# Kernel tuning notes

Hardware: AMD Instinct MI355X
Metric: run time of the kernel (lower is better)

Reference implementation:

```python
import math
import jax, jax.numpy as jnp
import numpy as np

B, H, L = 8, 512, 4096
N = 64 // 2  # d_state//2 complex pairs
DT_MIN, DT_MAX = 1e-3, 0.1


def setup_inputs() -> dict:
    key = jax.random.key(0)
    k_u, k_dt, k_C, k_D, k_W = jax.random.split(key, 5)
    u = jax.random.normal(k_u, (B, H, L), dtype=jnp.float32)
    log_dt = jax.random.uniform(k_dt, (H,), dtype=jnp.float32) * (
        math.log(DT_MAX) - math.log(DT_MIN)) + math.log(DT_MIN)
    log_A_real = jnp.log(0.5 * jnp.ones((H, N), dtype=jnp.float32))
    A_imag = math.pi * jnp.broadcast_to(jnp.arange(N, dtype=jnp.float32), (H, N))
    C = jax.random.normal(k_C, (H, N, 2), dtype=jnp.float32)  # view_as_real of cfloat
    D = jax.random.normal(k_D, (H,), dtype=jnp.float32)
    W_out = jax.random.normal(k_W, (2 * H, H), dtype=jnp.float32) * 0.05  # 1x1 conv weight
    b_out = jnp.zeros((2 * H,), dtype=jnp.float32)
    return {"u": u, "log_dt": log_dt, "log_A_real": log_A_real, "A_imag": A_imag,
            "C": C, "D": D, "W_out": W_out, "b_out": b_out}


def _ssm_kernel(log_dt, log_A_real, A_imag, C, length):
    dt = jnp.exp(log_dt)                             # (H,)
    A = -jnp.exp(log_A_real) + 1j * A_imag           # (H,N) complex
    dtA = A * dt[:, None]                            # (H,N)
    l = jnp.arange(length, dtype=jnp.float32)
    K = jnp.exp(dtA[:, :, None] * l)                 # (H,N,L) complex Vandermonde
    Cc = C[..., 0] + 1j * C[..., 1]                  # (H,N)
    Cs = Cc * (jnp.exp(dtA) - 1.0) / A               # (H,N)
    return 2.0 * jnp.einsum('hn,hnl->hl', Cs, K).real  # (H,L) real kernel


def reference(u, log_dt, log_A_real, A_imag, C, D, W_out, b_out):
    length = u.shape[-1]
    k = _ssm_kernel(log_dt, log_A_real, A_imag, C, length)  # (H,L)
    n_fft = 2 * length
    k_f = jnp.fft.rfft(k, n=n_fft)                   # (H, L+1)
    u_f = jnp.fft.rfft(u, n=n_fft)                   # (B,H,L+1)
    y = jnp.fft.irfft(u_f * k_f, n=n_fft)[..., :length]  # FFT convolution
    y = y + u * D[:, None]                           # D skip connection
    y = jax.nn.gelu(y, approximate=False)            # torch nn.GELU = exact erf
    y = jnp.einsum('oh,bhl->bol', W_out, y) + b_out[:, None]  # 1x1 conv
    a, b = jnp.split(y, 2, axis=-2)                  # GLU over channel dim
    return a * jax.nn.sigmoid(b)
```

## Files before the change

kernel.cpp:

```cpp
#include <hip/hip_runtime.h>
#include <math.h>

constexpr int cB = 8, cH = 512, cL = 4096, cN = 32;
constexpr int cG = 32, cLC = 128;
constexpr int cHN = cH * cN;

constexpr size_t OF_RR  = 0;
constexpr size_t OF_RI  = (size_t)cHN;
constexpr size_t OF_RPR = (size_t)2*cHN;
constexpr size_t OF_RPI = (size_t)3*cHN;
constexpr size_t OF_C2R = (size_t)4*cHN;
constexpr size_t OF_C2I = (size_t)5*cHN;
constexpr size_t OF_DR  = (size_t)6*cHN;
constexpr size_t OF_DI  = (size_t)7*cHN;
constexpr size_t OF_K   = (size_t)8*cHN;
constexpr size_t OF_WP  = OF_K + (size_t)512*128;
constexpr size_t OF_A   = OF_WP + (size_t)1024*512/2;
constexpr size_t OF_V   = OF_A + (size_t)512*128*192/2;
constexpr size_t OF_XP  = OF_V + (size_t)512*64*128/2;
constexpr size_t OF_G   = OF_XP + (size_t)512*256*64/2;

typedef __bf16 bf16x8 __attribute__((ext_vector_type(8)));
typedef float  f32x4  __attribute__((ext_vector_type(4)));

static __device__ __forceinline__ ushort f2bf(float x) {
    unsigned u = __float_as_uint(x);
    unsigned r = (u + 0x7fffu + ((u >> 16) & 1u)) >> 16;
    return (ushort)r;
}
static __device__ __forceinline__ float bf2f(ushort v) {
    return __uint_as_float(((unsigned)v) << 16);
}
static __device__ __forceinline__ unsigned pk2(float a, float b) {
    return (unsigned)f2bf(a) | ((unsigned)f2bf(b) << 16);
}
static __device__ __forceinline__ float gelu(float v) {
    return 0.5f * v * (1.0f + erff(v * 0.70710678118654752f));
}

__global__ void k_consts(const float* __restrict__ log_dt,
                         const float* __restrict__ log_A_real,
                         const float* __restrict__ A_imag,
                         const float* __restrict__ Cin,
                         float* __restrict__ ws)
{
    int tid = blockIdx.x * 256 + threadIdx.x;
    if (tid >= cHN) return;
    int h = tid >> 5;
    float dt = expf(log_dt[h]);
    float Ar = -expf(log_A_real[tid]);
    float Ai = A_imag[tid];
    float dr = dt * Ar, di = dt * Ai;
    float er = expf(dr);
    float rr = er * cosf(di), ri = er * sinf(di);
    float erL = expf(dr * (float)cLC);
    float diL = di * (float)cLC;
    float rpr = erL * cosf(diL), rpi = erL * sinf(diL);
    float cr = Cin[2*tid], ci = Cin[2*tid+1];
    float nr = rr - 1.0f, ni = ri;
    float inv = 1.0f / (Ar*Ar + Ai*Ai);
    float wr = (nr*Ar + ni*Ai) * inv;
    float wi = (ni*Ar - nr*Ai) * inv;
    float csr = cr*wr - ci*wi;
    float csi = cr*wi + ci*wr;
    ws[OF_RR  + tid] = rr;  ws[OF_RI  + tid] = ri;
    ws[OF_RPR + tid] = rpr; ws[OF_RPI + tid] = rpi;
    ws[OF_C2R + tid] = 2.0f*csr; ws[OF_C2I + tid] = 2.0f*csi;
    ws[OF_DR  + tid] = dr;  ws[OF_DI  + tid] = di;
}

__global__ void k_pack_w(const float* __restrict__ W, ushort* __restrict__ Wp)
{
    int idx = blockIdx.x * 256 + threadIdx.x;
    int base = idx * 4;
    int m = base >> 9;
    int k = base & 511;
    int src = (m & 1) ? (512 + (m >> 1)) : (m >> 1);
    float4 v = *(const float4*)&W[(size_t)src * 512 + k];
    ushort4 o;
    o.x = f2bf(v.x); o.y = f2bf(v.y); o.z = f2bf(v.z); o.w = f2bf(v.w);
    *(ushort4*)&Wp[base] = o;
}

__global__ void k_vmat(const float* __restrict__ ws, ushort* __restrict__ wsu)
{
    int tid = blockIdx.x * 256 + threadIdx.x;
    int h = tid >> 5, n = tid & 31;
    float dr = ws[OF_DR + tid], di = ws[OF_DI + tid];
    float e127 = expf(dr * 127.f), a127 = di * 127.f;
    float pr = e127 * cosf(a127), pi_ = e127 * sinf(a127);
    float rie = expf(-dr);
    float rc = rie * cosf(di), rs = -rie * sinf(di);
    ushort* vre = wsu + 2*OF_V + ((size_t)h*64 + n) * 128;
    ushort* vim = wsu + 2*OF_V + ((size_t)h*64 + 32 + n) * 128;
    for (int j4 = 0; j4 < 128; j4 += 4) {
        ushort4 r4, i4;
        #pragma unroll
        for (int e = 0; e < 4; ++e) {
            ((ushort*)&r4)[e] = f2bf(pr);
            ((ushort*)&i4)[e] = f2bf(pi_);
            float npr = pr*rc - pi_*rs;
            float npi = pr*rs + pi_*rc;
            pr = npr; pi_ = npi;
        }
        *(ushort4*)&vre[j4] = r4;
        *(ushort4*)&vim[j4] = i4;
    }
}

__global__ void k_emat(const float* __restrict__ ws, float* __restrict__ wsf,
                       ushort* __restrict__ wsu)
{
    int tid = blockIdx.x * 256 + threadIdx.x;
    int h = tid >> 7, l = tid & 127;
    float fl = (float)l, fl1 = (float)(l + 1);
    const float* dr_ = ws + OF_DR + (size_t)h*32;
    const float* di_ = ws + OF_DI + (size_t)h*32;
    const float* c2r_ = ws + OF_C2R + (size_t)h*32;
    const float* c2i_ = ws + OF_C2I + (size_t)h*32;
    ushort* rowA = wsu + 2*OF_A + ((size_t)h*128 + l) * 192;
    float kacc = 0.f;
    for (int n4 = 0; n4 < 32; n4 += 4) {
        ushort4 prq, npq;
        #pragma unroll
        for (int e = 0; e < 4; ++e) {
            int n = n4 + e;
            float dr = dr_[n], di = di_[n], c2r = c2r_[n], c2i = c2i_[n];
            float e0 = expf(dr * fl), a0 = di * fl;
            float c0 = cosf(a0), s0 = sinf(a0);
            kacc += e0 * (c2r*c0 - c2i*s0);
            float e1 = expf(dr * fl1), a1 = di * fl1;
            float c1 = cosf(a1), s1 = sinf(a1);
            ((ushort*)&prq)[e] = f2bf(e1 * (c2r*c1 - c2i*s1));
            ((ushort*)&npq)[e] = f2bf(-e1 * (c2r*s1 + c2i*c1));
        }
        *(ushort4*)&rowA[128 + n4] = prq;
        *(ushort4*)&rowA[160 + n4] = npq;
    }
    wsf[OF_K + (size_t)h*128 + l] = kacc;
}

__global__ void k_build_T(const float* __restrict__ wsf, const float* __restrict__ Dvec,
                          ushort* __restrict__ wsu)
{
    __shared__ float kv[256];
    int t = threadIdx.x;
    int tid = blockIdx.x * 256 + t;
    int h = tid >> 7, l = tid & 127;
    kv[t] = wsf[OF_K + (size_t)blockIdx.x * 256 + t];
    __syncthreads();
    const float* krow = kv + ((t >> 7) << 7);
    float Dh = Dvec[h];
    ushort* row = wsu + 2*OF_A + ((size_t)h*128 + l) * 192;
    for (int j8 = 0; j8 < 128; j8 += 8) {
        uint4 q;
        unsigned w[4];
        #pragma unroll
        for (int p = 0; p < 4; ++p) {
            int j0 = j8 + 2*p, j1 = j0 + 1;
            float v0 = (j0 <= l) ? krow[l - j0] : 0.f;
            float v1 = (j1 <= l) ? krow[l - j1] : 0.f;
            if (j0 == l) v0 += Dh;
            if (j1 == l) v1 += Dh;
            w[p] = pk2(v0, v1);
        }
        q.x = w[0]; q.y = w[1]; q.z = w[2]; q.w = w[3];
        *(uint4*)&row[j8] = q;
    }
}

__global__ __launch_bounds__(256) void k_state_gemm(const float* __restrict__ u,
                                                    const ushort* __restrict__ wsu,
                                                    ushort* __restrict__ xp)
{
    __shared__ ushort Vs[64 * 136];
    __shared__ ushort Bs[256 * 40];
    const int t = threadIdx.x;
    const int h = blockIdx.x;
    const int wn = t >> 6, lane = t & 63;
    const int lm = lane & 15, q = lane >> 4;

    {
        int idx = t * 32;
        int row = idx >> 7, kk = idx & 127;
        const ushort* src = wsu + 2*OF_V + ((size_t)h*64 + row) * 128 + kk;
        uint4 v0 = *(const uint4*)&src[0],  v1 = *(const uint4*)&src[8];
        uint4 v2 = *(const uint4*)&src[16], v3 = *(const uint4*)&src[24];
        ushort* d = (ushort*)Vs + row * 136 + kk;
        *(uint4*)&d[0] = v0; *(uint4*)&d[8] = v1;
        *(uint4*)&d[16] = v2; *(uint4*)&d[24] = v3;
    }

    const int b = t >> 5, c = t & 31;
    f32x4 acc[4][4];
    #pragma unroll
    for (int i = 0; i < 4; ++i)
        #pragma unroll
        for (int j = 0; j < 4; ++j) acc[i][j] = (f32x4){0.f,0.f,0.f,0.f};

    for (int k0 = 0; k0 < 128; k0 += 32) {
        const float* up = u + ((size_t)(b*cH + h)) * cL + (size_t)c*128 + k0;
        float4 f[8];
        #pragma unroll
        for (int e = 0; e < 8; ++e) f[e] = *(const float4*)&up[4*e];
        __syncthreads();
        ushort* d = (ushort*)Bs + t * 40;
        #pragma unroll
        for (int e = 0; e < 4; ++e) {
            uint4 w;
            w.x = pk2(f[2*e].x, f[2*e].y);   w.y = pk2(f[2*e].z, f[2*e].w);
            w.z = pk2(f[2*e+1].x, f[2*e+1].y); w.w = pk2(f[2*e+1].z, f[2*e+1].w);
            *(uint4*)&d[8*e] = w;
        }
        __syncthreads();
        bf16x8 af[4], bfr[4];
        #pragma unroll
        for (int mi = 0; mi < 4; ++mi)
            af[mi] = *(const bf16x8*)&Vs[(16*mi + lm) * 136 + k0 + 8*q];
        #pragma unroll
        for (int ni = 0; ni < 4; ++ni)
            bfr[ni] = *(const bf16x8*)&Bs[(64*wn + 16*ni + lm) * 40 + 8*q];
        #pragma unroll
        for (int mi = 0; mi < 4; ++mi)
            #pragma unroll
            for (int ni = 0; ni < 4; ++ni)
                acc[mi][ni] = __builtin_amdgcn_mfma_f32_16x16x32_bf16(af[mi], bfr[ni], acc[mi][ni], 0,0,0);
    }
    #pragma unroll
    for (int mi = 0; mi < 4; ++mi)
        #pragma unroll
        for (int ni = 0; ni < 4; ++ni) {
            int col = 64*wn + 16*ni + lm;
            int comp = 16*mi + 4*q;
            ushort4 st;
            st.x = f2bf(acc[mi][ni][0]); st.y = f2bf(acc[mi][ni][1]);
            st.z = f2bf(acc[mi][ni][2]); st.w = f2bf(acc[mi][ni][3]);
            *(ushort4*)&xp[((size_t)h*256 + col) * 64 + comp] = st;
        }
}

__global__ __launch_bounds__(256) void k_scan2(const float* __restrict__ ws,
                                               ushort* __restrict__ xp)
{
    int tid = blockIdx.x * 256 + threadIdx.x;
    int n  = tid & 31;
    int bh = tid >> 5;
    int h  = bh & (cH - 1);
    int b  = bh >> 9;
    float rpr = ws[OF_RPR + (size_t)h*32 + n];
    float rpi = ws[OF_RPI + (size_t)h*32 + n];
    float Xr = 0.f, Xi = 0.f;
    ushort* base = xp + ((size_t)h*256 + (size_t)b*32) * 64 + n;
    for (int c = 0; c < cG; ++c) {
        ushort* p = base + (size_t)c * 64;
        float sr = bf2f(p[0]), si = bf2f(p[32]);
        p[0]  = f2bf(Xr);
        p[32] = f2bf(Xi);
        float nXr = fmaf(rpr, Xr, fmaf(-rpi, Xi, sr));
        float nXi = fmaf(rpr, Xi, fmaf(rpi, Xr, si));
        Xr = nXr; Xi = nXi;
    }
}

__global__ __launch_bounds__(256) void k_conv(const float* __restrict__ u,
                                              const ushort* __restrict__ wsu,
                                              ushort* __restrict__ g)
{
    __shared__ ushort As[128 * 40];
    __shared__ ushort Bs[128 * 40];
    const int t = threadIdx.x;
    const int ctile = blockIdx.x;
    const int h = blockIdx.y;
    const int wave = t >> 6, lane = t & 63;
    const int wm = wave & 1, wn = wave >> 1;
    const int lm = lane & 15, q = lane >> 4;

    const int arow = t & 127, ah = t >> 7;
    const int col = arow, half = ah;
    const int gc = ctile * 128 + col;
    const int ub = gc >> 5, uc = gc & 31;

    const ushort* Ab = wsu + 2*OF_A + ((size_t)h*128 + arow) * 192;
    const ushort* xpB = wsu + 2*OF_XP + ((size_t)h*256 + gc) * 64;

    f32x4 acc[4][4];
    #pragma unroll
    for (int i = 0; i < 4; ++i)
        #pragma unroll
        for (int j = 0; j < 4; ++j) acc[i][j] = (f32x4){0.f,0.f,0.f,0.f};

    for (int k0 = 0; k0 < 192; k0 += 32) {
        uint4 a0 = *(const uint4*)&Ab[k0 + 16*ah];
        uint4 a1 = *(const uint4*)&Ab[k0 + 16*ah + 8];
        uint4 b0, b1;
        if (k0 < 128) {
            const float* up = u + ((size_t)(ub*cH + h)) * cL + (size_t)uc*128 + k0 + 16*half;
            float4 f0 = *(const float4*)&up[0],  f1 = *(const float4*)&up[4];
            float4 f2 = *(const float4*)&up[8],  f3 = *(const float4*)&up[12];
            b0.x = pk2(f0.x,f0.y); b0.y = pk2(f0.z,f0.w);
            b0.z = pk2(f1.x,f1.y); b0.w = pk2(f1.z,f1.w);
            b1.x = pk2(f2.x,f2.y); b1.y = pk2(f2.z,f2.w);
            b1.z = pk2(f3.x,f3.y); b1.w = pk2(f3.z,f3.w);
        } else {
            const ushort* xs = xpB + (k0 - 128) + 16*half;
            b0 = *(const uint4*)&xs[0];
            b1 = *(const uint4*)&xs[8];
        }
        __syncthreads();
        *(uint4*)&As[arow*40 + 16*ah]     = a0;
        *(uint4*)&As[arow*40 + 16*ah + 8] = a1;
        *(uint4*)&Bs[col*40 + 16*half]     = b0;
        *(uint4*)&Bs[col*40 + 16*half + 8] = b1;
        __syncthreads();
        bool skip = (wm == 0) && (k0 == 64 || k0 == 96);
        if (!skip) {
            bf16x8 af[4], bfr[4];
            #pragma unroll
            for (int mi = 0; mi < 4; ++mi)
                af[mi] = *(const bf16x8*)&As[(64*wm + 16*mi + lm) * 40 + 8*q];
            #pragma unroll
            for (int ni = 0; ni < 4; ++ni)
                bfr[ni] = *(const bf16x8*)&Bs[(64*wn + 16*ni + lm) * 40 + 8*q];
            #pragma unroll
            for (int mi = 0; mi < 4; ++mi)
                #pragma unroll
                for (int ni = 0; ni < 4; ++ni)
                    acc[mi][ni] = __builtin_amdgcn_mfma_f32_16x16x32_bf16(af[mi], bfr[ni], acc[mi][ni], 0,0,0);
        }
    }
    #pragma unroll
    for (int ni = 0; ni < 4; ++ni) {
        int ocol = ctile*128 + 64*wn + 16*ni + lm;
        int ob = ocol >> 5, oc = ocol & 31;
        ushort* grow = g + ((size_t)(ob*cH + h)) * cL + (size_t)oc*128;
        #pragma unroll
        for (int mi = 0; mi < 4; ++mi) {
            int l = 64*wm + 16*mi + 4*q;
            ushort4 st;
            st.x = f2bf(gelu(acc[mi][ni][0]));
            st.y = f2bf(gelu(acc[mi][ni][1]));
            st.z = f2bf(gelu(acc[mi][ni][2]));
            st.w = f2bf(gelu(acc[mi][ni][3]));
            *(ushort4*)&grow[l] = st;
        }
    }
}

constexpr int LDK = 40;
__global__ __launch_bounds__(256) void k_gemm_mfma(const ushort* __restrict__ Wp,
                                                   const float* __restrict__ bias,
                                                   const ushort* __restrict__ gbf,
                                                   float* __restrict__ out)
{
    __shared__ ushort As[128 * LDK];
    __shared__ ushort Bs[128 * LDK];
    const int t    = threadIdx.x;
    const int l0   = blockIdx.x * 128;
    const int by   = blockIdx.y;
    const int b    = blockIdx.z;
    const int wave = t >> 6, lane = t & 63;
    const int wm   = wave & 1, wn = wave >> 1;
    const int lm   = lane & 15, q = lane >> 4;

    const int arow = t & 127;
    const int ah   = t >> 7;
    const int lq = t & 15, kp = t >> 4;
    const int ko = kp >> 2;
    const int kr = (2 * kp) & 7;

    const ushort* gB = gbf + (size_t)b * ((size_t)cH * cL);
    const ushort* wRow = Wp + (size_t)(by * 128 + arow) * 512 + ah * 16;

    f32x4 acc[4][4];
    #pragma unroll
    for (int i = 0; i < 4; ++i)
        #pragma unroll
        for (int j = 0; j < 4; ++j)
            acc[i][j] = (f32x4){0.f, 0.f, 0.f, 0.f};

    for (int k0 = 0; k0 < cH; k0 += 32) {
        uint4 wa0 = *(const uint4*)&wRow[k0];
        uint4 wa1 = *(const uint4*)&wRow[k0 + 8];
        uint4 g0  = *(const uint4*)&gB[(size_t)(k0 + 2*kp)     * cL + l0 + 8*lq];
        uint4 g1  = *(const uint4*)&gB[(size_t)(k0 + 2*kp + 1) * cL + l0 + 8*lq];
        __syncthreads();
        *(uint4*)&As[arow * LDK + 16*ah]     = wa0;
        *(uint4*)&As[arow * LDK + 16*ah + 8] = wa1;
        {
            unsigned ua[4] = {g0.x, g0.y, g0.z, g0.w};
            unsigned ub[4] = {g1.x, g1.y, g1.z, g1.w};
            #pragma unroll
            for (int e = 0; e < 4; ++e) {
                unsigned w0 = (ua[e] & 0xffffu) | (ub[e] << 16);
                unsigned w1 = (ua[e] >> 16)     | (ub[e] & 0xffff0000u);
                int lr0 = 8*lq + 2*e;
                int c0  = ((ko ^ (lq & 3)) << 3) + kr;
                *(unsigned*)&Bs[lr0 * LDK + c0]       = w0;
                *(unsigned*)&Bs[(lr0 + 1) * LDK + c0] = w1;
            }
        }
        __syncthreads();
        bf16x8 af[4], bf[4];
        #pragma unroll
        for (int mi = 0; mi < 4; ++mi) {
            int row = 64*wm + 16*mi + lm;
            af[mi] = *(const bf16x8*)&As[row * LDK + (q << 3)];
        }
        #pragma unroll
        for (int ni = 0; ni < 4; ++ni) {
            int row = 64*wn + 16*ni + lm;
            int kx  = (row >> 3) & 3;
            bf[ni] = *(const bf16x8*)&Bs[row * LDK + ((q ^ kx) << 3)];
        }
        #pragma unroll
        for (int mi = 0; mi < 4; ++mi)
            #pragma unroll
            for (int ni = 0; ni < 4; ++ni)
                acc[mi][ni] = __builtin_amdgcn_mfma_f32_16x16x32_bf16(af[mi], bf[ni], acc[mi][ni], 0, 0, 0);
    }

    const int obase = by * 64 + 32 * wm;
    #pragma unroll
    for (int mi = 0; mi < 4; ++mi) {
        #pragma unroll
        for (int p = 0; p < 2; ++p) {
            int o = obase + 8*mi + 2*q + p;
            float ba = bias[o], bb = bias[512 + o];
            float* orow = out + ((size_t)b * cH + o) * cL + l0 + 64*wn + lm;
            #pragma unroll
            for (int ni = 0; ni < 4; ++ni) {
                float av = acc[mi][ni][2*p]     + ba;
                float gv = acc[mi][ni][2*p + 1] + bb;
                orow[16 * ni] = av / (1.f + expf(-gv));
            }
        }
    }
}

extern "C" void kernel_launch(void* const* d_in, const int* in_sizes, int n_in,
                              void* d_out, int out_size, void* d_ws, size_t ws_size,
                              hipStream_t stream)
{
    (void)in_sizes; (void)n_in; (void)out_size; (void)ws_size;
    const float* u          = (const float*)d_in[0];
    const float* log_dt     = (const float*)d_in[1];
    const float* log_A_real = (const float*)d_in[2];
    const float* A_imag     = (const float*)d_in[3];
    const float* C          = (const float*)d_in[4];
    const float* D          = (const float*)d_in[5];
    const float* W          = (const float*)d_in[6];
    const float* bias       = (const float*)d_in[7];
    float* out = (float*)d_out;
    float* ws  = (float*)d_ws;
    ushort* wsu = (ushort*)d_ws;
    ushort* Wp  = wsu + 2*OF_WP;
    ushort* xp  = wsu + 2*OF_XP;
    ushort* gbf = wsu + 2*OF_G;

    hipLaunchKernelGGL(k_consts, dim3(cHN/256), dim3(256), 0, stream,
                       log_dt, log_A_real, A_imag, C, ws);
    hipLaunchKernelGGL(k_pack_w, dim3(1024*512/4/256), dim3(256), 0, stream, W, Wp);
    hipLaunchKernelGGL(k_vmat, dim3(cHN/256), dim3(256), 0, stream, ws, wsu);
    hipLaunchKernelGGL(k_emat, dim3(512*128/256), dim3(256), 0, stream, ws, ws, wsu);
    hipLaunchKernelGGL(k_build_T, dim3(512*128/256), dim3(256), 0, stream, ws, D, wsu);
    hipLaunchKernelGGL(k_state_gemm, dim3(512), dim3(256), 0, stream, u, wsu, xp);
    hipLaunchKernelGGL(k_scan2, dim3(cB*cH*cN/256), dim3(256), 0, stream, ws, xp);
    hipLaunchKernelGGL(k_conv, dim3(2, 512), dim3(256), 0, stream, u, wsu, gbf);
    hipLaunchKernelGGL(k_gemm_mfma, dim3(cL/128, 1024/128, cB), dim3(256), 0, stream,
                       Wp, bias, gbf, out);
}
```

Before: 296.2 us.

## Fuse setup kernels, split state GEMM, transpose activations, enlarge output GEMM tile

Several preprocessing kernels are merged: the V-matrix build moves into the constants kernel, and the kernel-row computation feeds the Toeplitz build through shared memory instead of global memory. The state GEMM is split across two blocks per head to raise parallelism, and the scan keeps its 32-chunk state in registers. The final GEMM is replaced by an explicit transpose of the gelu activations into an L-major layout, followed by a larger-tile GEMM (128x256, K step 64) that loads contiguous rows without a register transpose. The transpose adds an extra pass over the activations, and the larger tiles raise register pressure.

New measurement: 384.3 us. 29.7% more time.

```diff
diff --git a/kernel.cpp b/kernel.cpp
--- a/kernel.cpp
+++ b/kernel.cpp
@@ -19,6 +19,7 @@
 constexpr size_t OF_V   = OF_A + (size_t)512*128*192/2;
 constexpr size_t OF_XP  = OF_V + (size_t)512*64*128/2;
 constexpr size_t OF_G   = OF_XP + (size_t)512*256*64/2;
+constexpr size_t OF_GT  = OF_A;
 
 typedef __bf16 bf16x8 __attribute__((ext_vector_type(8)));
 typedef float  f32x4  __attribute__((ext_vector_type(4)));
@@ -38,15 +39,15 @@
     return 0.5f * v * (1.0f + erff(v * 0.70710678118654752f));
 }
 
-__global__ void k_consts(const float* __restrict__ log_dt,
-                         const float* __restrict__ log_A_real,
-                         const float* __restrict__ A_imag,
-                         const float* __restrict__ Cin,
-                         float* __restrict__ ws)
+__global__ void k_init(const float* __restrict__ log_dt,
+                       const float* __restrict__ log_A_real,
+                       const float* __restrict__ A_imag,
+                       const float* __restrict__ Cin,
+                       float* __restrict__ ws, ushort* __restrict__ wsu)
 {
     int tid = blockIdx.x * 256 + threadIdx.x;
     if (tid >= cHN) return;
-    int h = tid >> 5;
+    int h = tid >> 5, n = tid & 31;
     float dt = expf(log_dt[h]);
     float Ar = -expf(log_A_real[tid]);
     float Ai = A_imag[tid];
@@ -67,6 +68,26 @@
     ws[OF_RPR + tid] = rpr; ws[OF_RPI + tid] = rpi;
     ws[OF_C2R + tid] = 2.0f*csr; ws[OF_C2I + tid] = 2.0f*csi;
     ws[OF_DR  + tid] = dr;  ws[OF_DI  + tid] = di;
+
+    float e127 = expf(dr * 127.f), a127 = di * 127.f;
+    float pr = e127 * cosf(a127), pi_ = e127 * sinf(a127);
+    float rie = expf(-dr);
+    float rc = rie * cosf(di), rs = -rie * sinf(di);
+    ushort* vre = wsu + 2*OF_V + ((size_t)h*64 + n) * 128;
+    ushort* vim = wsu + 2*OF_V + ((size_t)h*64 + 32 + n) * 128;
+    for (int j4 = 0; j4 < 128; j4 += 4) {
+        ushort4 r4, i4;
+        #pragma unroll
+        for (int e = 0; e < 4; ++e) {
+            ((ushort*)&r4)[e] = f2bf(pr);
+            ((ushort*)&i4)[e] = f2bf(pi_);
+            float npr = pr*rc - pi_*rs;
+            float npi = pr*rs + pi_*rc;
+            pr = npr; pi_ = npi;
+        }
+        *(ushort4*)&vre[j4] = r4;
+        *(ushort4*)&vim[j4] = i4;
+    }
 }
 
 __global__ void k_pack_w(const float* __restrict__ W, ushort* __restrict__ Wp)
@@ -82,37 +103,13 @@
     *(ushort4*)&Wp[base] = o;
 }
 
-__global__ void k_vmat(const float* __restrict__ ws, ushort* __restrict__ wsu)
-{
-    int tid = blockIdx.x * 256 + threadIdx.x;
-    int h = tid >> 5, n = tid & 31;
-    float dr = ws[OF_DR + tid], di = ws[OF_DI + tid];
-    float e127 = expf(dr * 127.f), a127 = di * 127.f;
-    float pr = e127 * cosf(a127), pi_ = e127 * sinf(a127);
-    float rie = expf(-dr);
-    float rc = rie * cosf(di), rs = -rie * sinf(di);
-    ushort* vre = wsu + 2*OF_V + ((size_t)h*64 + n) * 128;
-    ushort* vim = wsu + 2*OF_V + ((size_t)h*64 + 32 + n) * 128;
-    for (int j4 = 0; j4 < 128; j4 += 4) {
-        ushort4 r4, i4;
-        #pragma unroll
-        for (int e = 0; e < 4; ++e) {
-            ((ushort*)&r4)[e] = f2bf(pr);
-            ((ushort*)&i4)[e] = f2bf(pi_);
-            float npr = pr*rc - pi_*rs;
-            float npi = pr*rs + pi_*rc;
-            pr = npr; pi_ = npi;
-        }
-        *(ushort4*)&vre[j4] = r4;
-        *(ushort4*)&vim[j4] = i4;
-    }
-}
-
-__global__ void k_emat(const float* __restrict__ ws, float* __restrict__ wsf,
-                       ushort* __restrict__ wsu)
-{
-    int tid = blockIdx.x * 256 + threadIdx.x;
-    int h = tid >> 7, l = tid & 127;
+__global__ void k_ematT(const float* __restrict__ ws, const float* __restrict__ Dvec,
+                        ushort* __restrict__ wsu)
+{
+    __shared__ float kv[256];
+    int t = threadIdx.x;
+    int tid = blockIdx.x * 256 + t;
+    int h = tid >> 7, l = t & 127;
     float fl = (float)l, fl1 = (float)(l + 1);
     const float* dr_ = ws + OF_DR + (size_t)h*32;
     const float* di_ = ws + OF_DI + (size_t)h*32;
@@ -137,23 +134,12 @@
         *(ushort4*)&rowA[128 + n4] = prq;
         *(ushort4*)&rowA[160 + n4] = npq;
     }
-    wsf[OF_K + (size_t)h*128 + l] = kacc;
-}
-
-__global__ void k_build_T(const float* __restrict__ wsf, const float* __restrict__ Dvec,
-                          ushort* __restrict__ wsu)
-{
-    __shared__ float kv[256];
-    int t = threadIdx.x;
-    int tid = blockIdx.x * 256 + t;
-    int h = tid >> 7, l = tid & 127;
-    kv[t] = wsf[OF_K + (size_t)blockIdx.x * 256 + t];
+    kv[t] = kacc;
     __syncthreads();
     const float* krow = kv + ((t >> 7) << 7);
     float Dh = Dvec[h];
-    ushort* row = wsu + 2*OF_A + ((size_t)h*128 + l) * 192;
     for (int j8 = 0; j8 < 128; j8 += 8) {
-        uint4 q;
+        uint4 qv;
         unsigned w[4];
         #pragma unroll
         for (int p = 0; p < 4; ++p) {
@@ -164,8 +150,8 @@
             if (j1 == l) v1 += Dh;
             w[p] = pk2(v0, v1);
         }
-        q.x = w[0]; q.y = w[1]; q.z = w[2]; q.w = w[3];
-        *(uint4*)&row[j8] = q;
+        qv.x = w[0]; qv.y = w[1]; qv.z = w[2]; qv.w = w[3];
+        *(uint4*)&rowA[j8] = qv;
     }
 }
 
@@ -174,63 +160,62 @@
                                                     ushort* __restrict__ xp)
 {
     __shared__ ushort Vs[64 * 136];
-    __shared__ ushort Bs[256 * 40];
+    __shared__ ushort Bsm[128 * 40];
     const int t = threadIdx.x;
     const int h = blockIdx.x;
+    const int half = blockIdx.y;
     const int wn = t >> 6, lane = t & 63;
     const int lm = lane & 15, q = lane >> 4;
 
     {
-        int idx = t * 32;
-        int row = idx >> 7, kk = idx & 127;
-        const ushort* src = wsu + 2*OF_V + ((size_t)h*64 + row) * 128 + kk;
-        uint4 v0 = *(const uint4*)&src[0],  v1 = *(const uint4*)&src[8];
-        uint4 v2 = *(const uint4*)&src[16], v3 = *(const uint4*)&src[24];
-        ushort* d = (ushort*)Vs + row * 136 + kk;
-        *(uint4*)&d[0] = v0; *(uint4*)&d[8] = v1;
-        *(uint4*)&d[16] = v2; *(uint4*)&d[24] = v3;
-    }
-
-    const int b = t >> 5, c = t & 31;
-    f32x4 acc[4][4];
+        int row = t >> 2, seg = (t & 3) * 32;
+        const ushort* src = wsu + 2*OF_V + ((size_t)h*64 + row) * 128 + seg;
+        ushort* d = Vs + row * 136 + seg;
+        #pragma unroll
+        for (int i = 0; i < 4; ++i) *(uint4*)&d[8*i] = *(const uint4*)&src[8*i];
+    }
+
+    const int cl = t & 127;
+    const int gc = half * 128 + cl;
+    const int bb = gc >> 5, cc = gc & 31;
+    const int kh = (t >> 7) * 16;
+    f32x4 acc[4][2];
     #pragma unroll
     for (int i = 0; i < 4; ++i)
         #pragma unroll
-        for (int j = 0; j < 4; ++j) acc[i][j] = (f32x4){0.f,0.f,0.f,0.f};
+        for (int j = 0; j < 2; ++j) acc[i][j] = (f32x4){0.f,0.f,0.f,0.f};
 
     for (int k0 = 0; k0 < 128; k0 += 32) {
-        const float* up = u + ((size_t)(b*cH + h)) * cL + (size_t)c*128 + k0;
-        float4 f[8];
-        #pragma unroll
-        for (int e = 0; e < 8; ++e) f[e] = *(const float4*)&up[4*e];
-        __syncthreads();
-        ushort* d = (ushort*)Bs + t * 40;
-        #pragma unroll
-        for (int e = 0; e < 4; ++e) {
-            uint4 w;
-            w.x = pk2(f[2*e].x, f[2*e].y);   w.y = pk2(f[2*e].z, f[2*e].w);
-            w.z = pk2(f[2*e+1].x, f[2*e+1].y); w.w = pk2(f[2*e+1].z, f[2*e+1].w);
-            *(uint4*)&d[8*e] = w;
-        }
-        __syncthreads();
-        bf16x8 af[4], bfr[4];
+        const float* up = u + ((size_t)(bb*cH + h)) * cL + (size_t)cc*128 + k0 + kh;
+        float4 f0 = *(const float4*)&up[0],  f1 = *(const float4*)&up[4];
+        float4 f2 = *(const float4*)&up[8],  f3 = *(const float4*)&up[12];
+        __syncthreads();
+        ushort* d = Bsm + cl * 40 + kh;
+        uint4 w0, w1;
+        w0.x = pk2(f0.x,f0.y); w0.y = pk2(f0.z,f0.w);
+        w0.z = pk2(f1.x,f1.y); w0.w = pk2(f1.z,f1.w);
+        w1.x = pk2(f2.x,f2.y); w1.y = pk2(f2.z,f2.w);
+        w1.z = pk2(f3.x,f3.y); w1.w = pk2(f3.z,f3.w);
+        *(uint4*)&d[0] = w0; *(uint4*)&d[8] = w1;
+        __syncthreads();
+        bf16x8 af[4], bfr[2];
         #pragma unroll
         for (int mi = 0; mi < 4; ++mi)
             af[mi] = *(const bf16x8*)&Vs[(16*mi + lm) * 136 + k0 + 8*q];
         #pragma unroll
-        for (int ni = 0; ni < 4; ++ni)
-            bfr[ni] = *(const bf16x8*)&Bs[(64*wn + 16*ni + lm) * 40 + 8*q];
+        for (int ni = 0; ni < 2; ++ni)
+            bfr[ni] = *(const bf16x8*)&Bsm[(32*wn + 16*ni + lm) * 40 + 8*q];
         #pragma unroll
         for (int mi = 0; mi < 4; ++mi)
             #pragma unroll
-            for (int ni = 0; ni < 4; ++ni)
+            for (int ni = 0; ni < 2; ++ni)
                 acc[mi][ni] = __builtin_amdgcn_mfma_f32_16x16x32_bf16(af[mi], bfr[ni], acc[mi][ni], 0,0,0);
     }
     #pragma unroll
     for (int mi = 0; mi < 4; ++mi)
         #pragma unroll
-        for (int ni = 0; ni < 4; ++ni) {
-            int col = 64*wn + 16*ni + lm;
+        for (int ni = 0; ni < 2; ++ni) {
+            int col = half*128 + 32*wn + 16*ni + lm;
             int comp = 16*mi + 4*q;
             ushort4 st;
             st.x = f2bf(acc[mi][ni][0]); st.y = f2bf(acc[mi][ni][1]);
@@ -249,16 +234,26 @@
     int b  = bh >> 9;
     float rpr = ws[OF_RPR + (size_t)h*32 + n];
     float rpi = ws[OF_RPI + (size_t)h*32 + n];
+    ushort* base = xp + ((size_t)h*256 + (size_t)b*32) * 64 + n;
+    float sr[32], si[32];
+    #pragma unroll
+    for (int c = 0; c < 32; ++c) {
+        sr[c] = bf2f(base[(size_t)c*64]);
+        si[c] = bf2f(base[(size_t)c*64 + 32]);
+    }
     float Xr = 0.f, Xi = 0.f;
-    ushort* base = xp + ((size_t)h*256 + (size_t)b*32) * 64 + n;
-    for (int c = 0; c < cG; ++c) {
-        ushort* p = base + (size_t)c * 64;
-        float sr = bf2f(p[0]), si = bf2f(p[32]);
-        p[0]  = f2bf(Xr);
-        p[32] = f2bf(Xi);
-        float nXr = fmaf(rpr, Xr, fmaf(-rpi, Xi, sr));
-        float nXi = fmaf(rpr, Xi, fmaf(rpi, Xr, si));
+    #pragma unroll
+    for (int c = 0; c < 32; ++c) {
+        float tr = sr[c], ti = si[c];
+        sr[c] = Xr; si[c] = Xi;
+        float nXr = fmaf(rpr, Xr, fmaf(-rpi, Xi, tr));
+        float nXi = fmaf(rpr, Xi, fmaf(rpi, Xr, ti));
         Xr = nXr; Xi = nXi;
+    }
+    #pragma unroll
+    for (int c = 0; c < 32; ++c) {
+        base[(size_t)c*64]      = f2bf(sr[c]);
+        base[(size_t)c*64 + 32] = f2bf(si[c]);
     }
 }
 
@@ -346,89 +341,103 @@
     }
 }
 
-constexpr int LDK = 40;
-__global__ __launch_bounds__(256) void k_gemm_mfma(const ushort* __restrict__ Wp,
-                                                   const float* __restrict__ bias,
-                                                   const ushort* __restrict__ gbf,
-                                                   float* __restrict__ out)
-{
-    __shared__ ushort As[128 * LDK];
-    __shared__ ushort Bs[128 * LDK];
-    const int t    = threadIdx.x;
-    const int l0   = blockIdx.x * 128;
-    const int by   = blockIdx.y;
-    const int b    = blockIdx.z;
+__global__ __launch_bounds__(256) void k_tr(const ushort* __restrict__ g,
+                                            ushort* __restrict__ gT)
+{
+    __shared__ unsigned Ts[64 * 33];
+    const int t = threadIdx.x;
+    const int l0 = blockIdx.x * 64;
+    const int h0 = blockIdx.y * 64;
+    const int b  = blockIdx.z;
+    int hp = t >> 3, lseg = (t & 7) * 8;
+    const ushort* r0 = g + ((size_t)(b*cH + h0 + 2*hp) * cL + l0 + lseg);
+    const ushort* r1 = r0 + cL;
+    uint4 a = *(const uint4*)r0;
+    uint4 bq = *(const uint4*)r1;
+    const ushort* ap = (const ushort*)&a;
+    const ushort* bp = (const ushort*)&bq;
+    #pragma unroll
+    for (int j = 0; j < 8; ++j) {
+        unsigned w = (unsigned)ap[j] | ((unsigned)bp[j] << 16);
+        Ts[(lseg + j) * 33 + hp] = w;
+    }
+    __syncthreads();
+    int lr = t >> 2, hs = (t & 3) * 8;
+    unsigned v[8];
+    #pragma unroll
+    for (int i = 0; i < 8; ++i) v[i] = Ts[lr * 33 + hs + i];
+    uint4 o0, o1;
+    o0.x=v[0]; o0.y=v[1]; o0.z=v[2]; o0.w=v[3];
+    o1.x=v[4]; o1.y=v[5]; o1.z=v[6]; o1.w=v[7];
+    ushort* dst = gT + ((size_t)b * cL + l0 + lr) * cH + h0 + hs*2;
+    *(uint4*)&dst[0] = o0;
+    *(uint4*)&dst[8] = o1;
+}
+
+__global__ __launch_bounds__(256, 2) void k_gemm2(const ushort* __restrict__ Wp,
+                                                  const float* __restrict__ bias,
+                                                  const ushort* __restrict__ gT,
+                                                  float* __restrict__ out)
+{
+    __shared__ ushort As[128 * 72];
+    __shared__ ushort Bs[256 * 72];
+    const int t = threadIdx.x;
+    const int l0 = blockIdx.x * 256;
+    const int by = blockIdx.y;
+    const int b  = blockIdx.z;
     const int wave = t >> 6, lane = t & 63;
-    const int wm   = wave & 1, wn = wave >> 1;
-    const int lm   = lane & 15, q = lane >> 4;
-
-    const int arow = t & 127;
-    const int ah   = t >> 7;
-    const int lq = t & 15, kp = t >> 4;
-    const int ko = kp >> 2;
-    const int kr = (2 * kp) & 7;
-
-    const ushort* gB = gbf + (size_t)b * ((size_t)cH * cL);
-    const ushort* wRow = Wp + (size_t)(by * 128 + arow) * 512 + ah * 16;
-
-    f32x4 acc[4][4];
+    const int wm = wave & 1, wn = wave >> 1;
+    const int lm = lane & 15, q = lane >> 4;
+    const int arow = t & 127, ah = (t >> 7) * 32;
+
+    const ushort* wRow = Wp + (size_t)(by*128 + arow) * 512 + ah;
+    const ushort* gRow = gT + ((size_t)b * cL + l0 + t) * cH;
+
+    f32x4 acc[4][8];
     #pragma unroll
     for (int i = 0; i < 4; ++i)
         #pragma unroll
-        for (int j = 0; j < 4; ++j)
-            acc[i][j] = (f32x4){0.f, 0.f, 0.f, 0.f};
-
-    for (int k0 = 0; k0 < cH; k0 += 32) {
-        uint4 wa0 = *(const uint4*)&wRow[k0];
-        uint4 wa1 = *(const uint4*)&wRow[k0 + 8];
-        uint4 g0  = *(const uint4*)&gB[(size_t)(k0 + 2*kp)     * cL + l0 + 8*lq];
-        uint4 g1  = *(const uint4*)&gB[(size_t)(k0 + 2*kp + 1) * cL + l0 + 8*lq];
-        __syncthreads();
-        *(uint4*)&As[arow * LDK + 16*ah]     = wa0;
-        *(uint4*)&As[arow * LDK + 16*ah + 8] = wa1;
-        {
-            unsigned ua[4] = {g0.x, g0.y, g0.z, g0.w};
-            unsigned ub[4] = {g1.x, g1.y, g1.z, g1.w};
-            #pragma unroll
-            for (int e = 0; e < 4; ++e) {
-                unsigned w0 = (ua[e] & 0xffffu) | (ub[e] << 16);
-                unsigned w1 = (ua[e] >> 16)     | (ub[e] & 0xffff0000u);
-                int lr0 = 8*lq + 2*e;
-                int c0  = ((ko ^ (lq & 3)) << 3) + kr;
-                *(unsigned*)&Bs[lr0 * LDK + c0]       = w0;
-                *(unsigned*)&Bs[(lr0 + 1) * LDK + c0] = w1;
-            }
-        }
-        __syncthreads();
-        bf16x8 af[4], bf[4];
-        #pragma unroll
-        for (int mi = 0; mi < 4; ++mi) {
-            int row = 64*wm + 16*mi + lm;
-            af[mi] = *(const bf16x8*)&As[row * LDK + (q << 3)];
-        }
-        #pragma unroll
-        for (int ni = 0; ni < 4; ++ni) {
-            int row = 64*wn + 16*ni + lm;
-            int kx  = (row >> 3) & 3;
-            bf[ni] = *(const bf16x8*)&Bs[row * LDK + ((q ^ kx) << 3)];
-        }
-        #pragma unroll
-        for (int mi = 0; mi < 4; ++mi)
-            #pragma unroll
-            for (int ni = 0; ni < 4; ++ni)
-                acc[mi][ni] = __builtin_amdgcn_mfma_f32_16x16x32_bf16(af[mi], bf[ni], acc[mi][ni], 0, 0, 0);
-    }
-
-    const int obase = by * 64 + 32 * wm;
+        for (int j = 0; j < 8; ++j) acc[i][j] = (f32x4){0.f,0.f,0.f,0.f};
+
+    for (int k0 = 0; k0 < 512; k0 += 64) {
+        uint4 wa[4], gb[8];
+        #pragma unroll
+        for (int i = 0; i < 4; ++i) wa[i] = *(const uint4*)&wRow[k0 + 8*i];
+        #pragma unroll
+        for (int i = 0; i < 8; ++i) gb[i] = *(const uint4*)&gRow[k0 + 8*i];
+        __syncthreads();
+        #pragma unroll
+        for (int i = 0; i < 4; ++i) *(uint4*)&As[arow*72 + ah + 8*i] = wa[i];
+        #pragma unroll
+        for (int i = 0; i < 8; ++i) *(uint4*)&Bs[t*72 + 8*i] = gb[i];
+        __syncthreads();
+        #pragma unroll
+        for (int kk = 0; kk < 64; kk += 32) {
+            bf16x8 af[4], bfr[8];
+            #pragma unroll
+            for (int mi = 0; mi < 4; ++mi)
+                af[mi] = *(const bf16x8*)&As[(64*wm + 16*mi + lm)*72 + kk + 8*q];
+            #pragma unroll
+            for (int ni = 0; ni < 8; ++ni)
+                bfr[ni] = *(const bf16x8*)&Bs[(128*wn + 16*ni + lm)*72 + kk + 8*q];
+            #pragma unroll
+            for (int mi = 0; mi < 4; ++mi)
+                #pragma unroll
+                for (int ni = 0; ni < 8; ++ni)
+                    acc[mi][ni] = __builtin_amdgcn_mfma_f32_16x16x32_bf16(af[mi], bfr[ni], acc[mi][ni], 0,0,0);
+        }
+    }
+    const int obase = by*64 + 32*wm;
+    const int colb = l0 + 128*wn + lm;
     #pragma unroll
     for (int mi = 0; mi < 4; ++mi) {
         #pragma unroll
         for (int p = 0; p < 2; ++p) {
             int o = obase + 8*mi + 2*q + p;
             float ba = bias[o], bb = bias[512 + o];
-            float* orow = out + ((size_t)b * cH + o) * cL + l0 + 64*wn + lm;
-            #pragma unroll
-            for (int ni = 0; ni < 4; ++ni) {
+            float* orow = out + ((size_t)b * cH + o) * cL + colb;
+            #pragma unroll
+            for (int ni = 0; ni < 8; ++ni) {
                 float av = acc[mi][ni][2*p]     + ba;
                 float gv = acc[mi][ni][2*p + 1] + bb;
                 orow[16 * ni] = av / (1.f + expf(-gv));
@@ -456,16 +465,16 @@
     ushort* Wp  = wsu + 2*OF_WP;
     ushort* xp  = wsu + 2*OF_XP;
     ushort* gbf = wsu + 2*OF_G;
-
-    hipLaunchKernelGGL(k_consts, dim3(cHN/256), dim3(256), 0, stream,
-                       log_dt, log_A_real, A_imag, C, ws);
+    ushort* gT  = wsu + 2*OF_GT;
+
+    hipLaunchKernelGGL(k_init, dim3(cHN/256), dim3(256), 0, stream,
+                       log_dt, log_A_real, A_imag, C, ws, wsu);
     hipLaunchKernelGGL(k_pack_w, dim3(1024*512/4/256), dim3(256), 0, stream, W, Wp);
-    hipLaunchKernelGGL(k_vmat, dim3(cHN/256), dim3(256), 0, stream, ws, wsu);
-    hipLaunchKernelGGL(k_emat, dim3(512*128/256), dim3(256), 0, stream, ws, ws, wsu);
-    hipLaunchKernelGGL(k_build_T, dim3(512*128/256), dim3(256), 0, stream, ws, D, wsu);
-    hipLaunchKernelGGL(k_state_gemm, dim3(512), dim3(256), 0, stream, u, wsu, xp);
+    hipLaunchKernelGGL(k_ematT, dim3(512*128/256), dim3(256), 0, stream, ws, D, wsu);
+    hipLaunchKernelGGL(k_state_gemm, dim3(512, 2), dim3(256), 0, stream, u, wsu, xp);
     hipLaunchKernelGGL(k_scan2, dim3(cB*cH*cN/256), dim3(256), 0, stream, ws, xp);
     hipLaunchKernelGGL(k_conv, dim3(2, 512), dim3(256), 0, stream, u, wsu, gbf);
-    hipLaunchKernelGGL(k_gemm_mfma, dim3(cL/128, 1024/128, cB), dim3(256), 0, stream,
-                       Wp, bias, gbf, out);
-}
+    hipLaunchKernelGGL(k_tr, dim3(cL/64, cH/64, cB), dim3(256), 0, stream, gbf, gT);
+    hipLaunchKernelGGL(k_gemm2, dim3(cL/256, 1024/128, cB), dim3(256), 0, stream,
+                       Wp, bias, gT, out);
+}
```
